# Optimization experiments

Hardware: AMD Instinct MI355X
Metric: run time of the kernel (lower is better)

The kernel has to match this reference:

```python
import jax, jax.numpy as jnp
import numpy as np
import math

N_HEADS = 16

def setup_inputs() -> dict:
    key = jax.random.key(0)
    k1, k2, k3 = jax.random.split(key, 3)
    B, S, D = 2, 2048, 1024
    x = jax.random.normal(k1, (B, S, D), dtype=jnp.float32)
    qkv = 0.01 * jax.random.normal(k2, (3 * D, D), dtype=jnp.float32)
    wo = 0.01 * jax.random.normal(k3, (D, D), dtype=jnp.float32)
    return {"x": x, "qkv": qkv, "wo": wo}

def reference(x, qkv, wo):
    B, S, D = x.shape
    H = N_HEADS
    dh = D // H
    QKV = x @ qkv.T                      # [B,S,3D]
    Q, K, V = jnp.split(QKV, 3, axis=-1)
    q = Q.reshape(B, S, H, dh).transpose(0, 2, 1, 3)  # [B,H,S,dh]
    k = K.reshape(B, S, H, dh).transpose(0, 2, 1, 3)
    v = V.reshape(B, S, H, dh).transpose(0, 2, 1, 3)
    scores = jnp.einsum('bhqd,bhkd->bhqk', q, k) / math.sqrt(float(dh))
    # Faithful to original: multiply by lower-triangular mask, then set
    # exact zeros to -inf (masked positions become 0 then -inf).
    mask = jnp.tril(jnp.ones((S, S), dtype=scores.dtype))
    scores = scores * mask[None, None, :, :]
    scores = jnp.where(scores == 0, -jnp.inf, scores)
    attn = jax.nn.softmax(scores, axis=-1)
    out = jnp.einsum('bhqk,bhkd->bhqd', attn, v)       # [B,H,S,dh]
    out = out.transpose(0, 2, 1, 3).reshape(B, S, D)
    return out @ wo.T
```

## Files before the change

kernel.cpp:

```cpp
#include <hip/hip_runtime.h>

typedef unsigned short u16;
typedef unsigned int u32;
typedef __bf16 bf16x8 __attribute__((ext_vector_type(8)));
typedef float f32x4 __attribute__((ext_vector_type(4)));
typedef u16 u16x4 __attribute__((ext_vector_type(4)));

#define GL2LDS16(g, l)                                                         \
    __builtin_amdgcn_global_load_lds(                                          \
        (__attribute__((address_space(1))) const void*)(g),                    \
        (__attribute__((address_space(3))) void*)(l), 16, 0, 0)

#define SYNC_VM(n) asm volatile("s_waitcnt vmcnt(" #n ")\ns_barrier" ::: "memory")
#define BAR()      asm volatile("s_barrier" ::: "memory")

__device__ __forceinline__ u16 f2bf(float f) {
    union { float f; u32 u; } x; x.f = f;
    u32 r = x.u + 0x7FFFu + ((x.u >> 16) & 1u);
    return (u16)(r >> 16);
}

__global__ __launch_bounds__(256) void f32_to_bf16_kernel(const float* __restrict__ in,
                                                          u16* __restrict__ out, int n) {
    int i = (blockIdx.x * 256 + threadIdx.x) * 4;
    if (i >= n) return;
    float4 v = *(const float4*)(in + i);
    u16x4 o;
    o.x = f2bf(v.x); o.y = f2bf(v.y); o.z = f2bf(v.z); o.w = f2bf(v.w);
    *(u16x4*)(out + i) = o;
}

template <int TM, bool OUT_BF16>
__global__ __launch_bounds__(256) void gemm_bt(const u16* __restrict__ A,
                                               const u16* __restrict__ B,
                                               void* __restrict__ Cout,
                                               int M, int N, int K) {
    constexpr int MI = TM / 32;
    __shared__ u16 As[2][TM * 32];
    __shared__ u16 Bs[2][128 * 32];
    const int tid = threadIdx.x;
    const int w = tid >> 6, lane = tid & 63, ln = lane & 15, qd = lane >> 4;
    const int wr = w >> 1, wc = w & 1;
    const int m0 = blockIdx.y * TM, n0 = blockIdx.x * 128;

    const int srow = tid >> 2, scol = (tid & 3) * 8;
    const u16* Abase = A + (size_t)(m0 + srow) * K + scol;
    const u16* Bbase = B + (size_t)(n0 + srow) * K + scol;

    f32x4 acc[MI][4] = {};
    const int nsteps = K >> 5;

#pragma unroll
    for (int it = 0; it < TM / 64; ++it)
        GL2LDS16(Abase + (size_t)(it * 64) * K, &As[0][(tid + it * 256) * 8]);
#pragma unroll
    for (int it = 0; it < 2; ++it)
        GL2LDS16(Bbase + (size_t)(it * 64) * K, &Bs[0][(tid + it * 256) * 8]);

    for (int s = 0; s < nsteps; ++s) {
        const u16* Ab = As[s & 1];
        const u16* Bb = Bs[s & 1];
        if (s + 1 < nsteps) {
            const int nk = (s + 1) << 5;
            const int nb = (s + 1) & 1;
#pragma unroll
            for (int it = 0; it < TM / 64; ++it)
                GL2LDS16(Abase + (size_t)(it * 64) * K + nk, &As[nb][(tid + it * 256) * 8]);
#pragma unroll
            for (int it = 0; it < 2; ++it)
                GL2LDS16(Bbase + (size_t)(it * 64) * K + nk, &Bs[nb][(tid + it * 256) * 8]);
            if constexpr (TM == 128) SYNC_VM(4); else SYNC_VM(3);
        } else {
            SYNC_VM(0);
        }

        bf16x8 af[MI], bfr[4];
#pragma unroll
        for (int i = 0; i < MI; ++i)
            af[i] = *(const bf16x8*)&Ab[(wr * (TM / 2) + i * 16 + ln) * 32 + qd * 8];
#pragma unroll
        for (int j = 0; j < 4; ++j)
            bfr[j] = *(const bf16x8*)&Bb[(wc * 64 + j * 16 + ln) * 32 + qd * 8];
#pragma unroll
        for (int i = 0; i < MI; ++i)
#pragma unroll
            for (int j = 0; j < 4; ++j)
                acc[i][j] = __builtin_amdgcn_mfma_f32_16x16x32_bf16(af[i], bfr[j], acc[i][j], 0, 0, 0);
        BAR();
    }

#pragma unroll
    for (int i = 0; i < MI; ++i)
#pragma unroll
        for (int j = 0; j < 4; ++j)
#pragma unroll
            for (int r = 0; r < 4; ++r) {
                int row = m0 + wr * (TM / 2) + i * 16 + qd * 4 + r;
                int col = n0 + wc * 64 + j * 16 + ln;
                float v = acc[i][j][r];
                if constexpr (OUT_BF16)
                    ((u16*)Cout)[(size_t)row * N + col] = f2bf(v);
                else
                    ((float*)Cout)[(size_t)row * N + col] = v;
            }
}

__global__ __launch_bounds__(256) void vtrans_kernel(const u16* __restrict__ QKV,
                                                     u16* __restrict__ VtG) {
    __shared__ u16 T[64 * 72];
    const int tid = threadIdx.x;
    const int bh = blockIdx.y;
    const int b = bh >> 4, h = bh & 15;
    const int s0 = blockIdx.x * 64;
#pragma unroll
    for (int it = 0; it < 2; ++it) {
        int idx = it * 256 + tid;
        int sl = idx >> 3, dg = (idx & 7) << 3;
        union { uint4 v; u16 u[8]; } raw;
        raw.v = *(const uint4*)(QKV + (size_t)(b * 2048 + s0 + sl) * 3072 + 2048 + h * 64 + dg);
#pragma unroll
        for (int j = 0; j < 8; ++j) T[(dg + j) * 72 + sl] = raw.u[j];
    }
    __syncthreads();
#pragma unroll
    for (int it = 0; it < 2; ++it) {
        int idx = it * 256 + tid;
        int d = idx >> 3, sg = (idx & 7) << 3;
        *(uint4*)(VtG + ((size_t)(bh * 64 + d)) * 2048 + s0 + sg) = *(uint4*)&T[d * 72 + sg];
    }
}

__global__ __launch_bounds__(256) void attn_kernel(const u16* __restrict__ QKV,
                                                   const u16* __restrict__ VtG,
                                                   u16* __restrict__ AO) {
    __shared__ u16 Ks[2][64 * 64];
    __shared__ u16 Vts[2][64 * 64];
    __shared__ u16 Pls[4][16 * 64];

    const int tid = threadIdx.x;
    const int w = tid >> 6, lane = tid & 63, ln = lane & 15, qd = lane >> 4;
    const int b = blockIdx.z, h = blockIdx.y;
    const int qt = (int)gridDim.x - 1 - (int)blockIdx.x;
    const int q0 = qt * 64;
    const int myq = q0 + w * 16 + ln;
    const int bh = b * 16 + h;
    const int swz = ln & 7;
    const int nch = qt + 1;

    const int srow = tid >> 3;
    const int sgg = (tid & 7) ^ (srow & 7);
    const u16* ksrc = QKV + (size_t)(b * 2048 + srow) * 3072 + 1024 + h * 64 + sgg * 8;
    const u16* vsrc = VtG + (size_t)(bh * 64 + srow) * 2048 + sgg * 8;

    GL2LDS16(ksrc, &Ks[0][tid * 8]);
    GL2LDS16(ksrc + (size_t)32 * 3072, &Ks[0][tid * 8 + 2048]);
    GL2LDS16(vsrc, &Vts[0][tid * 8]);
    GL2LDS16(vsrc + (size_t)32 * 2048, &Vts[0][tid * 8 + 2048]);

    const u16* qp = QKV + (size_t)(b * 2048 + myq) * 3072 + h * 64;
    bf16x8 qf0 = *(const bf16x8*)(qp + qd * 8);
    bf16x8 qf1 = *(const bf16x8*)(qp + 32 + qd * 8);

    f32x4 o[4] = {};
    float l_part = 0.f;
    u16* Pw = Pls[w];

    for (int c = 0; c < nch; ++c) {
        if (c + 1 < nch) {
            const int k1 = (c + 1) * 64;
            const int nb = (c + 1) & 1;
            GL2LDS16(ksrc + (size_t)k1 * 3072, &Ks[nb][tid * 8]);
            GL2LDS16(ksrc + (size_t)(k1 + 32) * 3072, &Ks[nb][tid * 8 + 2048]);
            GL2LDS16(vsrc + k1, &Vts[nb][tid * 8]);
            GL2LDS16(vsrc + k1 + 32 * 2048, &Vts[nb][tid * 8 + 2048]);
            SYNC_VM(4);
        } else {
            SYNC_VM(0);
        }
        const u16* Kb = Ks[c & 1];
        const u16* Vb = Vts[c & 1];

        f32x4 s[4];
#pragma unroll
        for (int kt = 0; kt < 4; ++kt) {
            const u16* kr = Kb + (kt * 16 + ln) * 64;
            bf16x8 kf0 = *(const bf16x8*)(kr + ((qd ^ swz) * 8));
            bf16x8 kf1 = *(const bf16x8*)(kr + (((qd + 4) ^ swz) * 8));
            f32x4 z = {0.f, 0.f, 0.f, 0.f};
            z = __builtin_amdgcn_mfma_f32_16x16x32_bf16(kf0, qf0, z, 0, 0, 0);
            z = __builtin_amdgcn_mfma_f32_16x16x32_bf16(kf1, qf1, z, 0, 0, 0);
            s[kt] = z;
        }

        if (c == nch - 1) {
#pragma unroll
            for (int kt = 0; kt < 4; ++kt)
#pragma unroll
                for (int r = 0; r < 4; ++r) {
                    int key = q0 + kt * 16 + qd * 4 + r;
                    float v = s[kt][r] * 0.125f;
                    s[kt][r] = (key > myq) ? -1e30f : v;
                }
        } else {
#pragma unroll
            for (int kt = 0; kt < 4; ++kt)
#pragma unroll
                for (int r = 0; r < 4; ++r) s[kt][r] *= 0.125f;
        }
#pragma unroll
        for (int kt = 0; kt < 4; ++kt)
#pragma unroll
            for (int r = 0; r < 4; ++r) {
                float p = __expf(s[kt][r]);
                s[kt][r] = p;
                l_part += p;
            }

#pragma unroll
        for (int kt = 0; kt < 4; ++kt) {
            u16x4 pk;
            pk.x = f2bf(s[kt][0]); pk.y = f2bf(s[kt][1]);
            pk.z = f2bf(s[kt][2]); pk.w = f2bf(s[kt][3]);
            int g = kt * 2 + (qd >> 1);
            *(u16x4*)&Pw[ln * 64 + ((g ^ swz) * 8) + (qd & 1) * 4] = pk;
        }
        bf16x8 pf0 = *(const bf16x8*)&Pw[ln * 64 + ((qd ^ swz) * 8)];
        bf16x8 pf1 = *(const bf16x8*)&Pw[ln * 64 + (((qd + 4) ^ swz) * 8)];

#pragma unroll
        for (int dt = 0; dt < 4; ++dt) {
            const u16* vr = Vb + (dt * 16 + ln) * 64;
            bf16x8 vf0 = *(const bf16x8*)(vr + ((qd ^ swz) * 8));
            bf16x8 vf1 = *(const bf16x8*)(vr + (((qd + 4) ^ swz) * 8));
            o[dt] = __builtin_amdgcn_mfma_f32_16x16x32_bf16(vf0, pf0, o[dt], 0, 0, 0);
            o[dt] = __builtin_amdgcn_mfma_f32_16x16x32_bf16(vf1, pf1, o[dt], 0, 0, 0);
        }
        BAR();
    }

    float l = l_part;
    l += __shfl_xor(l, 16);
    l += __shfl_xor(l, 32);
    float inv = 1.0f / l;
#pragma unroll
    for (int dt = 0; dt < 4; ++dt) {
        u16x4 ov;
        ov.x = f2bf(o[dt][0] * inv); ov.y = f2bf(o[dt][1] * inv);
        ov.z = f2bf(o[dt][2] * inv); ov.w = f2bf(o[dt][3] * inv);
        *(u16x4*)&AO[(size_t)(b * 2048 + myq) * 1024 + h * 64 + dt * 16 + qd * 4] = ov;
    }
}

extern "C" void kernel_launch(void* const* d_in, const int* in_sizes, int n_in,
                              void* d_out, int out_size, void* d_ws, size_t ws_size,
                              hipStream_t stream) {
    const float* x   = (const float*)d_in[0];
    const float* qkv = (const float*)d_in[1];
    const float* wo  = (const float*)d_in[2];
    float* out = (float*)d_out;

    char* ws = (char*)d_ws;
    u16* xb   = (u16*)(ws + 0);
    u16* qkvb = (u16*)(ws + 8388608);
    u16* wob  = (u16*)(ws + 14680064);
    u16* QKVo = (u16*)(ws + 16777216);
    u16* AO   = (u16*)(ws + 41943040);
    u16* VtG  = (u16*)(ws + 0);

    f32_to_bf16_kernel<<<4096, 256, 0, stream>>>(x,   xb,   4194304);
    f32_to_bf16_kernel<<<3072, 256, 0, stream>>>(qkv, qkvb, 3145728);
    f32_to_bf16_kernel<<<1024, 256, 0, stream>>>(wo,  wob,  1048576);

    gemm_bt<128, true><<<dim3(24, 32), 256, 0, stream>>>(xb, qkvb, QKVo, 4096, 3072, 1024);

    vtrans_kernel<<<dim3(32, 32), 256, 0, stream>>>(QKVo, VtG);

    attn_kernel<<<dim3(32, 16, 2), 256, 0, stream>>>(QKVo, VtG, AO);

    gemm_bt<64, false><<<dim3(8, 64), 256, 0, stream>>>(AO, wob, out, 4096, 1024, 1024);
}
```

Before: 204.9 us.

## Pair causal query tiles per attention block and merge conversion launches

```diff
diff --git a/kernel.cpp b/kernel.cpp
--- a/kernel.cpp
+++ b/kernel.cpp
@@ -20,11 +20,17 @@
     return (u16)(r >> 16);
 }
 
-__global__ __launch_bounds__(256) void f32_to_bf16_kernel(const float* __restrict__ in,
-                                                          u16* __restrict__ out, int n) {
+__global__ __launch_bounds__(256) void convert_all_kernel(const float* __restrict__ x,
+                                                          const float* __restrict__ qkv,
+                                                          const float* __restrict__ wo,
+                                                          u16* __restrict__ out) {
     int i = (blockIdx.x * 256 + threadIdx.x) * 4;
-    if (i >= n) return;
-    float4 v = *(const float4*)(in + i);
+    const float* src;
+    int off;
+    if (i < 4194304)      { src = x;   off = i; }
+    else if (i < 7340032) { src = qkv; off = i - 4194304; }
+    else                  { src = wo;  off = i - 7340032; }
+    float4 v = *(const float4*)(src + off);
     u16x4 o;
     o.x = f2bf(v.x); o.y = f2bf(v.y); o.z = f2bf(v.z); o.w = f2bf(v.w);
     *(u16x4*)(out + i) = o;
@@ -135,17 +141,18 @@
                                                    u16* __restrict__ AO) {
     __shared__ u16 Ks[2][64 * 64];
     __shared__ u16 Vts[2][64 * 64];
-    __shared__ u16 Pls[4][16 * 64];
+    __shared__ u16 Pls[4][2][16 * 64];
 
     const int tid = threadIdx.x;
     const int w = tid >> 6, lane = tid & 63, ln = lane & 15, qd = lane >> 4;
     const int b = blockIdx.z, h = blockIdx.y;
-    const int qt = (int)gridDim.x - 1 - (int)blockIdx.x;
-    const int q0 = qt * 64;
-    const int myq = q0 + w * 16 + ln;
+    const int qtA = blockIdx.x;
+    const int qtB = 31 - qtA;
+    const int myqA = qtA * 64 + w * 16 + ln;
+    const int myqB = qtB * 64 + w * 16 + ln;
     const int bh = b * 16 + h;
     const int swz = ln & 7;
-    const int nch = qt + 1;
+    const int nch = qtB + 1;
 
     const int srow = tid >> 3;
     const int sgg = (tid & 7) ^ (srow & 7);
@@ -157,13 +164,17 @@
     GL2LDS16(vsrc, &Vts[0][tid * 8]);
     GL2LDS16(vsrc + (size_t)32 * 2048, &Vts[0][tid * 8 + 2048]);
 
-    const u16* qp = QKV + (size_t)(b * 2048 + myq) * 3072 + h * 64;
-    bf16x8 qf0 = *(const bf16x8*)(qp + qd * 8);
-    bf16x8 qf1 = *(const bf16x8*)(qp + 32 + qd * 8);
-
-    f32x4 o[4] = {};
-    float l_part = 0.f;
-    u16* Pw = Pls[w];
+    const u16* qpA = QKV + (size_t)(b * 2048 + myqA) * 3072 + h * 64;
+    const u16* qpB = QKV + (size_t)(b * 2048 + myqB) * 3072 + h * 64;
+    bf16x8 qfA0 = *(const bf16x8*)(qpA + qd * 8);
+    bf16x8 qfA1 = *(const bf16x8*)(qpA + 32 + qd * 8);
+    bf16x8 qfB0 = *(const bf16x8*)(qpB + qd * 8);
+    bf16x8 qfB1 = *(const bf16x8*)(qpB + 32 + qd * 8);
+
+    f32x4 oA[4] = {}, oB[4] = {};
+    float lA = 0.f, lB = 0.f;
+    u16* PwA = &Pls[w][0][0];
+    u16* PwB = &Pls[w][1][0];
 
     for (int c = 0; c < nch; ++c) {
         if (c + 1 < nch) {
@@ -179,75 +190,112 @@
         }
         const u16* Kb = Ks[c & 1];
         const u16* Vb = Vts[c & 1];
-
-        f32x4 s[4];
+        const bool actA = (c <= qtA);
+
+        f32x4 sA[4], sB[4];
 #pragma unroll
         for (int kt = 0; kt < 4; ++kt) {
             const u16* kr = Kb + (kt * 16 + ln) * 64;
             bf16x8 kf0 = *(const bf16x8*)(kr + ((qd ^ swz) * 8));
             bf16x8 kf1 = *(const bf16x8*)(kr + (((qd + 4) ^ swz) * 8));
             f32x4 z = {0.f, 0.f, 0.f, 0.f};
-            z = __builtin_amdgcn_mfma_f32_16x16x32_bf16(kf0, qf0, z, 0, 0, 0);
-            z = __builtin_amdgcn_mfma_f32_16x16x32_bf16(kf1, qf1, z, 0, 0, 0);
-            s[kt] = z;
-        }
-
-        if (c == nch - 1) {
+            z = __builtin_amdgcn_mfma_f32_16x16x32_bf16(kf0, qfB0, z, 0, 0, 0);
+            z = __builtin_amdgcn_mfma_f32_16x16x32_bf16(kf1, qfB1, z, 0, 0, 0);
+            sB[kt] = z;
+            if (actA) {
+                f32x4 y = {0.f, 0.f, 0.f, 0.f};
+                y = __builtin_amdgcn_mfma_f32_16x16x32_bf16(kf0, qfA0, y, 0, 0, 0);
+                y = __builtin_amdgcn_mfma_f32_16x16x32_bf16(kf1, qfA1, y, 0, 0, 0);
+                sA[kt] = y;
+            }
+        }
+
+        if (c == qtB) {
 #pragma unroll
             for (int kt = 0; kt < 4; ++kt)
 #pragma unroll
                 for (int r = 0; r < 4; ++r) {
-                    int key = q0 + kt * 16 + qd * 4 + r;
-                    float v = s[kt][r] * 0.125f;
-                    s[kt][r] = (key > myq) ? -1e30f : v;
+                    int key = c * 64 + kt * 16 + qd * 4 + r;
+                    float v = sB[kt][r] * 0.125f;
+                    sB[kt][r] = (key > myqB) ? -1e30f : v;
                 }
         } else {
 #pragma unroll
             for (int kt = 0; kt < 4; ++kt)
 #pragma unroll
-                for (int r = 0; r < 4; ++r) s[kt][r] *= 0.125f;
-        }
-#pragma unroll
-        for (int kt = 0; kt < 4; ++kt)
-#pragma unroll
-            for (int r = 0; r < 4; ++r) {
-                float p = __expf(s[kt][r]);
-                s[kt][r] = p;
-                l_part += p;
-            }
-
+                for (int r = 0; r < 4; ++r) sB[kt][r] *= 0.125f;
+        }
 #pragma unroll
         for (int kt = 0; kt < 4; ++kt) {
             u16x4 pk;
-            pk.x = f2bf(s[kt][0]); pk.y = f2bf(s[kt][1]);
-            pk.z = f2bf(s[kt][2]); pk.w = f2bf(s[kt][3]);
+            float p0 = __expf(sB[kt][0]), p1 = __expf(sB[kt][1]);
+            float p2 = __expf(sB[kt][2]), p3 = __expf(sB[kt][3]);
+            lB += p0 + p1 + p2 + p3;
+            pk.x = f2bf(p0); pk.y = f2bf(p1); pk.z = f2bf(p2); pk.w = f2bf(p3);
             int g = kt * 2 + (qd >> 1);
-            *(u16x4*)&Pw[ln * 64 + ((g ^ swz) * 8) + (qd & 1) * 4] = pk;
-        }
-        bf16x8 pf0 = *(const bf16x8*)&Pw[ln * 64 + ((qd ^ swz) * 8)];
-        bf16x8 pf1 = *(const bf16x8*)&Pw[ln * 64 + (((qd + 4) ^ swz) * 8)];
+            *(u16x4*)&PwB[ln * 64 + ((g ^ swz) * 8) + (qd & 1) * 4] = pk;
+        }
+        bf16x8 pfB0 = *(const bf16x8*)&PwB[ln * 64 + ((qd ^ swz) * 8)];
+        bf16x8 pfB1 = *(const bf16x8*)&PwB[ln * 64 + (((qd + 4) ^ swz) * 8)];
+
+        bf16x8 pfA0, pfA1;
+        if (actA) {
+            if (c == qtA) {
+#pragma unroll
+                for (int kt = 0; kt < 4; ++kt)
+#pragma unroll
+                    for (int r = 0; r < 4; ++r) {
+                        int key = c * 64 + kt * 16 + qd * 4 + r;
+                        float v = sA[kt][r] * 0.125f;
+                        sA[kt][r] = (key > myqA) ? -1e30f : v;
+                    }
+            } else {
+#pragma unroll
+                for (int kt = 0; kt < 4; ++kt)
+#pragma unroll
+                    for (int r = 0; r < 4; ++r) sA[kt][r] *= 0.125f;
+            }
+#pragma unroll
+            for (int kt = 0; kt < 4; ++kt) {
+                u16x4 pk;
+                float p0 = __expf(sA[kt][0]), p1 = __expf(sA[kt][1]);
+                float p2 = __expf(sA[kt][2]), p3 = __expf(sA[kt][3]);
+                lA += p0 + p1 + p2 + p3;
+                pk.x = f2bf(p0); pk.y = f2bf(p1); pk.z = f2bf(p2); pk.w = f2bf(p3);
+                int g = kt * 2 + (qd >> 1);
+                *(u16x4*)&PwA[ln * 64 + ((g ^ swz) * 8) + (qd & 1) * 4] = pk;
+            }
+            pfA0 = *(const bf16x8*)&PwA[ln * 64 + ((qd ^ swz) * 8)];
+            pfA1 = *(const bf16x8*)&PwA[ln * 64 + (((qd + 4) ^ swz) * 8)];
+        }
 
 #pragma unroll
         for (int dt = 0; dt < 4; ++dt) {
             const u16* vr = Vb + (dt * 16 + ln) * 64;
             bf16x8 vf0 = *(const bf16x8*)(vr + ((qd ^ swz) * 8));
             bf16x8 vf1 = *(const bf16x8*)(vr + (((qd + 4) ^ swz) * 8));
-            o[dt] = __builtin_amdgcn_mfma_f32_16x16x32_bf16(vf0, pf0, o[dt], 0, 0, 0);
-            o[dt] = __builtin_amdgcn_mfma_f32_16x16x32_bf16(vf1, pf1, o[dt], 0, 0, 0);
+            oB[dt] = __builtin_amdgcn_mfma_f32_16x16x32_bf16(vf0, pfB0, oB[dt], 0, 0, 0);
+            oB[dt] = __builtin_amdgcn_mfma_f32_16x16x32_bf16(vf1, pfB1, oB[dt], 0, 0, 0);
+            if (actA) {
+                oA[dt] = __builtin_amdgcn_mfma_f32_16x16x32_bf16(vf0, pfA0, oA[dt], 0, 0, 0);
+                oA[dt] = __builtin_amdgcn_mfma_f32_16x16x32_bf16(vf1, pfA1, oA[dt], 0, 0, 0);
+            }
         }
         BAR();
     }
 
-    float l = l_part;
-    l += __shfl_xor(l, 16);
-    l += __shfl_xor(l, 32);
-    float inv = 1.0f / l;
+    lA += __shfl_xor(lA, 16); lA += __shfl_xor(lA, 32);
+    lB += __shfl_xor(lB, 16); lB += __shfl_xor(lB, 32);
+    float invA = 1.0f / lA, invB = 1.0f / lB;
 #pragma unroll
     for (int dt = 0; dt < 4; ++dt) {
         u16x4 ov;
-        ov.x = f2bf(o[dt][0] * inv); ov.y = f2bf(o[dt][1] * inv);
-        ov.z = f2bf(o[dt][2] * inv); ov.w = f2bf(o[dt][3] * inv);
-        *(u16x4*)&AO[(size_t)(b * 2048 + myq) * 1024 + h * 64 + dt * 16 + qd * 4] = ov;
+        ov.x = f2bf(oA[dt][0] * invA); ov.y = f2bf(oA[dt][1] * invA);
+        ov.z = f2bf(oA[dt][2] * invA); ov.w = f2bf(oA[dt][3] * invA);
+        *(u16x4*)&AO[(size_t)(b * 2048 + myqA) * 1024 + h * 64 + dt * 16 + qd * 4] = ov;
+        ov.x = f2bf(oB[dt][0] * invB); ov.y = f2bf(oB[dt][1] * invB);
+        ov.z = f2bf(oB[dt][2] * invB); ov.w = f2bf(oB[dt][3] * invB);
+        *(u16x4*)&AO[(size_t)(b * 2048 + myqB) * 1024 + h * 64 + dt * 16 + qd * 4] = ov;
     }
 }
 
@@ -267,15 +315,13 @@
     u16* AO   = (u16*)(ws + 41943040);
     u16* VtG  = (u16*)(ws + 0);
 
-    f32_to_bf16_kernel<<<4096, 256, 0, stream>>>(x,   xb,   4194304);
-    f32_to_bf16_kernel<<<3072, 256, 0, stream>>>(qkv, qkvb, 3145728);
-    f32_to_bf16_kernel<<<1024, 256, 0, stream>>>(wo,  wob,  1048576);
+    convert_all_kernel<<<8192, 256, 0, stream>>>(x, qkv, wo, xb);
 
     gemm_bt<128, true><<<dim3(24, 32), 256, 0, stream>>>(xb, qkvb, QKVo, 4096, 3072, 1024);
 
     vtrans_kernel<<<dim3(32, 32), 256, 0, stream>>>(QKVo, VtG);
 
-    attn_kernel<<<dim3(32, 16, 2), 256, 0, stream>>>(QKVo, VtG, AO);
+    attn_kernel<<<dim3(16, 16, 2), 256, 0, stream>>>(QKVo, VtG, AO);
 
     gemm_bt<64, false><<<dim3(8, 64), 256, 0, stream>>>(AO, wob, out, 4096, 1024, 1024);
 }
```

New measurement: 192.7 us. 1.06x faster.
